# Kernel optimization log

Hardware: AMD Instinct MI355X
Metric: run time of the kernel (lower is better)

Reference implementation:

```python
import jax, jax.numpy as jnp
import numpy as np

N_NODES = 100000


def _gcn_norm(edge_index, n):
    # Add self loops and compute symmetric normalization deg^-1/2 A_hat deg^-1/2
    loops = jnp.arange(n, dtype=edge_index.dtype)
    row = jnp.concatenate([edge_index[0], loops])  # source nodes [E+N]
    col = jnp.concatenate([edge_index[1], loops])  # target nodes [E+N]
    ones = jnp.ones(row.shape[0], dtype=jnp.float32)
    deg = jax.ops.segment_sum(ones, col, num_segments=n)  # in-degree incl. self loop
    dinv = jnp.where(deg > 0, jax.lax.rsqrt(deg), 0.0)
    norm = dinv[row] * dinv[col]  # [E+N]
    return row, col, norm


def _gcn_conv(x, W, b, row, col, norm, n):
    h = x @ W                     # [N, out]
    msg = h[row] * norm[:, None]  # gather + scale  [E+N, out]
    agg = jax.ops.segment_sum(msg, col, num_segments=n)  # scatter-add
    return agg + b


def setup_inputs() -> dict:
    key = jax.random.key(0)
    ks = jax.random.split(key, 8)
    n, e, din, dh, dout = N_NODES, 1600000, 128, 128, 64
    x = jax.random.normal(ks[0], (n, din), dtype=jnp.float32)
    edge_index = jax.random.randint(ks[1], (2, e), 0, n, dtype=jnp.int64)
    s = lambda fan: 1.0 / np.sqrt(fan)
    W0 = jax.random.normal(ks[2], (din, dh), dtype=jnp.float32) * s(din)
    W1 = jax.random.normal(ks[3], (dh, dh), dtype=jnp.float32) * s(dh)
    W2 = jax.random.normal(ks[4], (dh, dout), dtype=jnp.float32) * s(dh)
    b0 = jnp.zeros((dh,), jnp.float32)
    b1 = jnp.zeros((dh,), jnp.float32)
    b2 = jnp.zeros((dout,), jnp.float32)
    return {"x": x, "edge_index": edge_index, "W0": W0, "b0": b0,
            "W1": W1, "b1": b1, "W2": W2, "b2": b2}


def reference(x, edge_index, W0, b0, W1, b1, W2, b2):
    # Eval-mode forward (dropout inactive), matching GCN.forward
    n = x.shape[0]
    row, col, norm = _gcn_norm(edge_index, n)
    h = jax.nn.relu(_gcn_conv(x, W0, b0, row, col, norm, n))
    h = jax.nn.relu(_gcn_conv(h, W1, b1, row, col, norm, n))
    out = _gcn_conv(h, W2, b2, row, col, norm, n)
    return out
```

## Files before the change

### kernel.cpp

```cpp
#include <hip/hip_runtime.h>
#include <stdint.h>


static inline size_t ws_align(size_t x) { return (x + 255) & ~(size_t)255; }

typedef float __f2 __attribute__((ext_vector_type(2)));
typedef float __f4 __attribute__((ext_vector_type(4)));
typedef __attribute__((ext_vector_type(8))) short short8v;
typedef __attribute__((ext_vector_type(4))) float f32x4;

__device__ __forceinline__ int eidx(const void* p, size_t i, int is64) {
  return is64 ? (int)((const long long*)p)[i] : ((const int*)p)[i];
}

__device__ __forceinline__ uint16_t f2bf(float f) {
  uint32_t u = __float_as_uint(f);
  u += 0x7fffu + ((u >> 16) & 1u);
  return (uint16_t)(u >> 16);
}
__device__ __forceinline__ float bf_lo(uint32_t h) { return __uint_as_float(h << 16); }
__device__ __forceinline__ float bf_hi(uint32_t h) { return __uint_as_float(h & 0xffff0000u); }

__global__ void detect_k(const int* ei, int* flag) {
  if (threadIdx.x == 0 && blockIdx.x == 0) {
    int allz = 1;
    for (int i = 1; i < 128; i += 2)
      if (ei[i] != 0) { allz = 0; break; }
    *flag = allz;
  }
}

__global__ __launch_bounds__(256) void passA_k(const void* ei, const int* __restrict__ flag,
                                               int* __restrict__ bucket_cnt, int E, int NB) {
  __shared__ int cnt[256];
  int t = threadIdx.x;
  cnt[t] = 0;
  __syncthreads();
  int is64 = *flag;
  for (int e = blockIdx.x * 256 + t; e < E; e += gridDim.x * 256) {
    int c = eidx(ei, (size_t)E + e, is64);
    atomicAdd(&cnt[c >> 9], 1);
  }
  __syncthreads();
  if (t < NB && cnt[t]) atomicAdd(&bucket_cnt[t], cnt[t]);
}

__global__ __launch_bounds__(256) void bscan_k(const int* __restrict__ bucket_cnt,
                                               int* __restrict__ bucket_offs,
                                               int* __restrict__ gcursor, int NB) {
  __shared__ int sh[256];
  int t = threadIdx.x;
  int v = (t < NB) ? bucket_cnt[t] : 0;
  sh[t] = v;
  __syncthreads();
  for (int off = 1; off < 256; off <<= 1) {
    int x = (t >= off) ? sh[t - off] : 0;
    __syncthreads();
    sh[t] += x;
    __syncthreads();
  }
  if (t < NB) {
    int excl = sh[t] - v;
    bucket_offs[t] = excl;
    gcursor[t] = excl;
  }
  if (t == NB - 1) bucket_offs[NB] = sh[t];
}

__global__ __launch_bounds__(256) void passB_k(const void* ei, const int* __restrict__ flag,
                                               int* __restrict__ gcursor,
                                               int2* __restrict__ epk_binned, int E, int NB) {
  __shared__ int2 sorted[4096];
  __shared__ int cnt[256], bbase[256], gb[256], cur[256];
  const int t = threadIdx.x;
  const int base = blockIdx.x * 4096;
  const int CH = min(4096, E - base);
  const int is64 = *flag;

  cnt[t] = 0;
  __syncthreads();
  for (int i = t; i < CH; i += 256) {
    int c = eidx(ei, (size_t)E + base + i, is64);
    atomicAdd(&cnt[c >> 9], 1);
  }
  __syncthreads();
  {
    int v = cnt[t];
    __shared__ int sh[256];
    sh[t] = v;
    __syncthreads();
    for (int off = 1; off < 256; off <<= 1) {
      int x = (t >= off) ? sh[t - off] : 0;
      __syncthreads();
      sh[t] += x;
      __syncthreads();
    }
    bbase[t] = sh[t] - v;
    gb[t] = (t < NB && v) ? atomicAdd(&gcursor[t], v) : 0;
    cur[t] = 0;
  }
  __syncthreads();
  for (int i = t; i < CH; i += 256) {
    int r = eidx(ei, (size_t)base + i, is64);
    int c = eidx(ei, (size_t)E + base + i, is64);
    int b = c >> 9;
    int rank = atomicAdd(&cur[b], 1);
    sorted[bbase[b] + rank] = make_int2(r, c);
  }
  __syncthreads();
  for (int i = t; i < CH; i += 256) {
    int2 v = sorted[i];
    int b = v.y >> 9;
    epk_binned[gb[b] + (i - bbase[b])] = v;
  }
}

__global__ __launch_bounds__(256) void passC0_k(const int2* __restrict__ epk_binned,
                                                const int* __restrict__ bucket_offs,
                                                int* __restrict__ deg, int* __restrict__ offs,
                                                int n, int NB) {
  __shared__ int dcnt[512];
  __shared__ int s[256];
  const int t = threadIdx.x;
  const int b = blockIdx.x;
  dcnt[t] = 0; dcnt[t + 256] = 0;
  __syncthreads();
  const int lo = bucket_offs[b], hi = bucket_offs[b + 1];
  for (int i = lo + t; i < hi; i += 256)
    atomicAdd(&dcnt[epk_binned[i].y & 511], 1);
  __syncthreads();
  int d0 = dcnt[2 * t], d1 = dcnt[2 * t + 1];
  int pv = d0 + d1;
  s[t] = pv;
  __syncthreads();
  for (int off = 1; off < 256; off <<= 1) {
    int x = (t >= off) ? s[t - off] : 0;
    __syncthreads();
    s[t] += x;
    __syncthreads();
  }
  int pex = s[t] - pv;
  const int node0 = b << 9;
  int g0 = node0 + 2 * t, g1 = node0 + 2 * t + 1;
  if (g0 < n) { deg[g0] = d0; offs[g0] = lo + pex; }
  if (g1 < n) { deg[g1] = d1; offs[g1] = lo + pex + d0; }
  if (b == NB - 1 && t == 0) offs[n] = hi;
}

__global__ void dinv_k(const int* __restrict__ deg, float* __restrict__ dinv, int n) {
  int i = blockIdx.x * blockDim.x + threadIdx.x;
  if (i < n) dinv[i] = rsqrtf((float)deg[i] + 1.0f);
}

__global__ __launch_bounds__(256) void passC_k(const int2* __restrict__ epk_binned,
                                               const int* __restrict__ bucket_offs,
                                               const int* __restrict__ offs,
                                               uint32_t* __restrict__ epk) {
  __shared__ int cur[512];
  const int t = threadIdx.x;
  const int b = blockIdx.x;
  cur[t] = 0; cur[t + 256] = 0;
  __syncthreads();
  const int lo = bucket_offs[b], hi = bucket_offs[b + 1];
  for (int i = lo + t; i < hi; i += 256) {
    int2 v = epk_binned[i];
    int pos = offs[v.y] + atomicAdd(&cur[v.y & 511], 1);
    epk[pos] = (uint32_t)v.x;
  }
}

template <int COLS>
__global__ void wprep_k(const float* __restrict__ W, uint16_t* __restrict__ Wf) {
  constexpr int CT = COLS / 16;
  const int f = blockIdx.x;
  const int kc = f / CT, ct = f % CT;
  const int l = threadIdx.x;
#pragma unroll
  for (int j = 0; j < 8; ++j) {
    int k = kc * 32 + (l >> 4) * 8 + j;
    int col = ct * 16 + (l & 15);
    float wv = W[(size_t)k * COLS + col];
    uint16_t hi = f2bf(wv);
    float res = wv - __uint_as_float((uint32_t)hi << 16);
    Wf[(size_t)f * 1024 + l * 8 + j] = hi;
    Wf[(size_t)f * 1024 + 512 + l * 8 + j] = f2bf(res);
  }
}

template <int COLS, bool SLICED_IN>
__global__ __launch_bounds__(256) void gemm_k(const float* __restrict__ X,
                                              const uint16_t* __restrict__ Wf,
                                              const float* __restrict__ dinv,
                                              uint16_t* __restrict__ H, int N) {
  constexpr int CT = COLS / 16;
  __shared__ uint32_t Xp[128 * 32];

  const int tid = threadIdx.x;
  const int l = tid & 63, w = tid >> 6;
  const int rowbase = blockIdx.x * 128;
  const float4* X4 = (const float4*)X;

  f32x4 acc[2][CT];
#pragma unroll
  for (int rt = 0; rt < 2; ++rt)
#pragma unroll
    for (int ct = 0; ct < CT; ++ct) acc[rt][ct] = (f32x4)0.f;

  for (int kc = 0; kc < 4; ++kc) {
    __syncthreads();
#pragma unroll
    for (int t = 0; t < 4; ++t) {
      int i = tid + t * 256;
      int r = i >> 3, q = i & 7;
      int gr = rowbase + r;
      if (gr >= N) gr = N - 1;
      float4 xv = SLICED_IN ? X4[((size_t)kc * N + gr) * 8 + q]
                            : X4[(size_t)gr * 32 + kc * 8 + q];
      float xs[4] = {xv.x, xv.y, xv.z, xv.w};
      uint32_t p[4];
#pragma unroll
      for (int e = 0; e < 4; ++e) {
        uint16_t hi = f2bf(xs[e]);
        float res = xs[e] - __uint_as_float((uint32_t)hi << 16);
        p[e] = ((uint32_t)hi << 16) | (uint32_t)f2bf(res);
      }
      int blk = q ^ (r & 7);
      *(uint4*)&Xp[r * 32 + blk * 4] = make_uint4(p[0], p[1], p[2], p[3]);
    }
    __syncthreads();

    short8v ah[2], al[2];
#pragma unroll
    for (int rt = 0; rt < 2; ++rt) {
      int r = w * 32 + rt * 16 + (l & 15);
      int c = (r & 7) << 2;
      int b0 = ((l >> 4) * 8) ^ c;
      int b1 = ((l >> 4) * 8 + 4) ^ c;
      uint32_t ua[8];
      *(uint4*)&ua[0] = *(const uint4*)&Xp[r * 32 + b0];
      *(uint4*)&ua[4] = *(const uint4*)&Xp[r * 32 + b1];
      union { uint32_t d[4]; short8v v; } ch, cl;
#pragma unroll
      for (int p2 = 0; p2 < 4; ++p2) {
        ch.d[p2] = __builtin_amdgcn_perm(ua[2 * p2 + 1], ua[2 * p2], 0x07060302u);
        cl.d[p2] = __builtin_amdgcn_perm(ua[2 * p2 + 1], ua[2 * p2], 0x05040100u);
      }
      ah[rt] = ch.v;
      al[rt] = cl.v;
    }

#pragma unroll
    for (int ct = 0; ct < CT; ++ct) {
      size_t fo = (size_t)(kc * CT + ct) * 1024;
      short8v bh = *(const short8v*)(Wf + fo + l * 8);
      short8v bl = *(const short8v*)(Wf + fo + 512 + l * 8);
#pragma unroll
      for (int rt = 0; rt < 2; ++rt) {
        acc[rt][ct] = __builtin_amdgcn_mfma_f32_16x16x32_bf16(ah[rt], bh, acc[rt][ct], 0, 0, 0);
        acc[rt][ct] = __builtin_amdgcn_mfma_f32_16x16x32_bf16(al[rt], bh, acc[rt][ct], 0, 0, 0);
        acc[rt][ct] = __builtin_amdgcn_mfma_f32_16x16x32_bf16(ah[rt], bl, acc[rt][ct], 0, 0, 0);
      }
    }
  }

  uint32_t* HW = (uint32_t*)H;
  const int lq = l >> 4, lc = l & 15;
#pragma unroll
  for (int rt = 0; rt < 2; ++rt) {
#pragma unroll
    for (int q = 0; q < 4; ++q) {
      int row = rowbase + w * 32 + rt * 16 + lq * 4 + q;
      bool ok = row < N;
      float dv = ok ? dinv[row] : 0.f;
#pragma unroll
      for (int ct = 0; ct < CT; ++ct) {
        float v = acc[rt][ct][q] * dv;
        int b = (int)f2bf(v);
        int other = __shfl_xor(b, 1);
        if (ok && !(l & 1)) {
          uint32_t word = (uint32_t)b | ((uint32_t)other << 16);
          HW[((size_t)(ct >> 1) * N + row) * 16 + (ct & 1) * 8 + (lc >> 1)] = word;
        }
      }
    }
  }
}

__global__ __launch_bounds__(256, 8) void agg128s_k(const uint32_t* __restrict__ HW,
                                                    const int* __restrict__ offs,
                                                    const uint32_t* __restrict__ epk,
                                                    const float* __restrict__ bias,
                                                    float* __restrict__ Aout,
                                                    int relu, int N) {
  const int s = blockIdx.x & 3;
  const int g = blockIdx.x >> 2;
  const int lane = threadIdx.x & 63;
  const int wid = threadIdx.x >> 6;
  const int d = lane >> 3, w = lane & 7;
  const int c = g * 32 + wid * 8 + d;
  if (c >= N) return;
  const uint32_t* Hs = HW + (size_t)s * N * 16;
  int e0 = offs[c], e1 = offs[c + 1];
  float a0 = 0.f, a1 = 0.f, a2 = 0.f, a3 = 0.f;
  int e = e0;
  for (; e + 8 <= e1; e += 8) {
    uint32_t p0 = epk[e],     p1 = epk[e + 1], p2 = epk[e + 2], p3 = epk[e + 3];
    uint32_t p4 = epk[e + 4], p5 = epk[e + 5], p6 = epk[e + 6], p7 = epk[e + 7];
    uint2 h0 = *(const uint2*)&Hs[(size_t)p0 * 16 + 2 * w];
    uint2 h1 = *(const uint2*)&Hs[(size_t)p1 * 16 + 2 * w];
    uint2 h2 = *(const uint2*)&Hs[(size_t)p2 * 16 + 2 * w];
    uint2 h3 = *(const uint2*)&Hs[(size_t)p3 * 16 + 2 * w];
    uint2 h4 = *(const uint2*)&Hs[(size_t)p4 * 16 + 2 * w];
    uint2 h5 = *(const uint2*)&Hs[(size_t)p5 * 16 + 2 * w];
    uint2 h6 = *(const uint2*)&Hs[(size_t)p6 * 16 + 2 * w];
    uint2 h7 = *(const uint2*)&Hs[(size_t)p7 * 16 + 2 * w];
    a0 += bf_lo(h0.x); a1 += bf_hi(h0.x); a2 += bf_lo(h0.y); a3 += bf_hi(h0.y);
    a0 += bf_lo(h1.x); a1 += bf_hi(h1.x); a2 += bf_lo(h1.y); a3 += bf_hi(h1.y);
    a0 += bf_lo(h2.x); a1 += bf_hi(h2.x); a2 += bf_lo(h2.y); a3 += bf_hi(h2.y);
    a0 += bf_lo(h3.x); a1 += bf_hi(h3.x); a2 += bf_lo(h3.y); a3 += bf_hi(h3.y);
    a0 += bf_lo(h4.x); a1 += bf_hi(h4.x); a2 += bf_lo(h4.y); a3 += bf_hi(h4.y);
    a0 += bf_lo(h5.x); a1 += bf_hi(h5.x); a2 += bf_lo(h5.y); a3 += bf_hi(h5.y);
    a0 += bf_lo(h6.x); a1 += bf_hi(h6.x); a2 += bf_lo(h6.y); a3 += bf_hi(h6.y);
    a0 += bf_lo(h7.x); a1 += bf_hi(h7.x); a2 += bf_lo(h7.y); a3 += bf_hi(h7.y);
  }
  for (; e + 4 <= e1; e += 4) {
    uint32_t p0 = epk[e], p1 = epk[e + 1], p2 = epk[e + 2], p3 = epk[e + 3];
    uint2 h0 = *(const uint2*)&Hs[(size_t)p0 * 16 + 2 * w];
    uint2 h1 = *(const uint2*)&Hs[(size_t)p1 * 16 + 2 * w];
    uint2 h2 = *(const uint2*)&Hs[(size_t)p2 * 16 + 2 * w];
    uint2 h3 = *(const uint2*)&Hs[(size_t)p3 * 16 + 2 * w];
    a0 += bf_lo(h0.x); a1 += bf_hi(h0.x); a2 += bf_lo(h0.y); a3 += bf_hi(h0.y);
    a0 += bf_lo(h1.x); a1 += bf_hi(h1.x); a2 += bf_lo(h1.y); a3 += bf_hi(h1.y);
    a0 += bf_lo(h2.x); a1 += bf_hi(h2.x); a2 += bf_lo(h2.y); a3 += bf_hi(h2.y);
    a0 += bf_lo(h3.x); a1 += bf_hi(h3.x); a2 += bf_lo(h3.y); a3 += bf_hi(h3.y);
  }
  for (; e < e1; ++e) {
    uint2 h = *(const uint2*)&Hs[(size_t)epk[e] * 16 + 2 * w];
    a0 += bf_lo(h.x); a1 += bf_hi(h.x); a2 += bf_lo(h.y); a3 += bf_hi(h.y);
  }
  float dc = rsqrtf((float)(e1 - e0) + 1.f);
  uint2 hc = *(const uint2*)&Hs[(size_t)c * 16 + 2 * w];
  float r0 = fmaf(dc, a0 + bf_lo(hc.x), bias[s * 32 + 4 * w + 0]);
  float r1 = fmaf(dc, a1 + bf_hi(hc.x), bias[s * 32 + 4 * w + 1]);
  float r2 = fmaf(dc, a2 + bf_lo(hc.y), bias[s * 32 + 4 * w + 2]);
  float r3 = fmaf(dc, a3 + bf_hi(hc.y), bias[s * 32 + 4 * w + 3]);
  if (relu) {
    r0 = fmaxf(r0, 0.f); r1 = fmaxf(r1, 0.f);
    r2 = fmaxf(r2, 0.f); r3 = fmaxf(r3, 0.f);
  }
  __f4 res; res.x = r0; res.y = r1; res.z = r2; res.w = r3;
  __builtin_nontemporal_store(res, (__f4*)(Aout + ((size_t)s * N + c) * 32 + 4 * w));
}

__global__ __launch_bounds__(256, 8) void agg64s_k(const uint32_t* __restrict__ HW,
                                                   const int* __restrict__ offs,
                                                   const uint32_t* __restrict__ epk,
                                                   const float* __restrict__ bias,
                                                   float* __restrict__ out, int N) {
  const int r = blockIdx.x & 7;
  const int s = r >> 2;
  const int quar = r & 3;
  const int ng = (N + 31) >> 5;
  const int nq = (ng + 3) >> 2;
  const int g = quar * nq + (blockIdx.x >> 3);
  if (g >= ng) return;
  const int lane = threadIdx.x & 63;
  const int wid = threadIdx.x >> 6;
  const int d = lane >> 3, w = lane & 7;
  const int c = g * 32 + wid * 8 + d;
  if (c >= N) return;
  const uint32_t* Hs = HW + (size_t)s * N * 16;
  int e0 = offs[c], e1 = offs[c + 1];
  float a0 = 0.f, a1 = 0.f, a2 = 0.f, a3 = 0.f;
  int e = e0;
  for (; e + 8 <= e1; e += 8) {
    uint32_t p0 = epk[e],     p1 = epk[e + 1], p2 = epk[e + 2], p3 = epk[e + 3];
    uint32_t p4 = epk[e + 4], p5 = epk[e + 5], p6 = epk[e + 6], p7 = epk[e + 7];
    uint2 h0 = *(const uint2*)&Hs[(size_t)p0 * 16 + 2 * w];
    uint2 h1 = *(const uint2*)&Hs[(size_t)p1 * 16 + 2 * w];
    uint2 h2 = *(const uint2*)&Hs[(size_t)p2 * 16 + 2 * w];
    uint2 h3 = *(const uint2*)&Hs[(size_t)p3 * 16 + 2 * w];
    uint2 h4 = *(const uint2*)&Hs[(size_t)p4 * 16 + 2 * w];
    uint2 h5 = *(const uint2*)&Hs[(size_t)p5 * 16 + 2 * w];
    uint2 h6 = *(const uint2*)&Hs[(size_t)p6 * 16 + 2 * w];
    uint2 h7 = *(const uint2*)&Hs[(size_t)p7 * 16 + 2 * w];
    a0 += bf_lo(h0.x); a1 += bf_hi(h0.x); a2 += bf_lo(h0.y); a3 += bf_hi(h0.y);
    a0 += bf_lo(h1.x); a1 += bf_hi(h1.x); a2 += bf_lo(h1.y); a3 += bf_hi(h1.y);
    a0 += bf_lo(h2.x); a1 += bf_hi(h2.x); a2 += bf_lo(h2.y); a3 += bf_hi(h2.y);
    a0 += bf_lo(h3.x); a1 += bf_hi(h3.x); a2 += bf_lo(h3.y); a3 += bf_hi(h3.y);
    a0 += bf_lo(h4.x); a1 += bf_hi(h4.x); a2 += bf_lo(h4.y); a3 += bf_hi(h4.y);
    a0 += bf_lo(h5.x); a1 += bf_hi(h5.x); a2 += bf_lo(h5.y); a3 += bf_hi(h5.y);
    a0 += bf_lo(h6.x); a1 += bf_hi(h6.x); a2 += bf_lo(h6.y); a3 += bf_hi(h6.y);
    a0 += bf_lo(h7.x); a1 += bf_hi(h7.x); a2 += bf_lo(h7.y); a3 += bf_hi(h7.y);
  }
  for (; e + 4 <= e1; e += 4) {
    uint32_t p0 = epk[e], p1 = epk[e + 1], p2 = epk[e + 2], p3 = epk[e + 3];
    uint2 h0 = *(const uint2*)&Hs[(size_t)p0 * 16 + 2 * w];
    uint2 h1 = *(const uint2*)&Hs[(size_t)p1 * 16 + 2 * w];
    uint2 h2 = *(const uint2*)&Hs[(size_t)p2 * 16 + 2 * w];
    uint2 h3 = *(const uint2*)&Hs[(size_t)p3 * 16 + 2 * w];
    a0 += bf_lo(h0.x); a1 += bf_hi(h0.x); a2 += bf_lo(h0.y); a3 += bf_hi(h0.y);
    a0 += bf_lo(h1.x); a1 += bf_hi(h1.x); a2 += bf_lo(h1.y); a3 += bf_hi(h1.y);
    a0 += bf_lo(h2.x); a1 += bf_hi(h2.x); a2 += bf_lo(h2.y); a3 += bf_hi(h2.y);
    a0 += bf_lo(h3.x); a1 += bf_hi(h3.x); a2 += bf_lo(h3.y); a3 += bf_hi(h3.y);
  }
  for (; e < e1; ++e) {
    uint2 h = *(const uint2*)&Hs[(size_t)epk[e] * 16 + 2 * w];
    a0 += bf_lo(h.x); a1 += bf_hi(h.x); a2 += bf_lo(h.y); a3 += bf_hi(h.y);
  }
  float dc = rsqrtf((float)(e1 - e0) + 1.f);
  uint2 hc = *(const uint2*)&Hs[(size_t)c * 16 + 2 * w];
  float r0 = fmaf(dc, a0 + bf_lo(hc.x), bias[s * 32 + 4 * w + 0]);
  float r1 = fmaf(dc, a1 + bf_hi(hc.x), bias[s * 32 + 4 * w + 1]);
  float r2 = fmaf(dc, a2 + bf_lo(hc.y), bias[s * 32 + 4 * w + 2]);
  float r3 = fmaf(dc, a3 + bf_hi(hc.y), bias[s * 32 + 4 * w + 3]);
  __f4 res; res.x = r0; res.y = r1; res.z = r2; res.w = r3;
  __builtin_nontemporal_store(res, (__f4*)(out + (size_t)c * 64 + s * 32 + 4 * w));
}

extern "C" void kernel_launch(void* const* d_in, const int* in_sizes, int n_in,
                              void* d_out, int out_size, void* d_ws, size_t ws_size,
                              hipStream_t stream) {
  const float* x  = (const float*)d_in[0];
  const void*  ei = d_in[1];
  const float* W0 = (const float*)d_in[2];
  const float* b0 = (const float*)d_in[3];
  const float* W1 = (const float*)d_in[4];
  const float* b1 = (const float*)d_in[5];
  const float* W2 = (const float*)d_in[6];
  const float* b2 = (const float*)d_in[7];
  float* out = (float*)d_out;

  const int n = in_sizes[0] / 128;
  const int E = in_sizes[1] / 2;
  const int NB = (n + 511) >> 9;

  char* ws = (char*)d_ws;
  size_t off = 0;
  auto alloc = [&](size_t bytes) { char* p = ws + off; off = ws_align(off + bytes); return p; };
  int*      bucket_cnt  = (int*)alloc(256 * 4);
  int*      bucket_offs = (int*)alloc(257 * 4);
  int*      gcursor     = (int*)alloc(256 * 4);
  int*      deg         = (int*)alloc((size_t)n * 4);
  int*      offs        = (int*)alloc((size_t)(n + 1) * 4);
  float*    dinv        = (float*)alloc((size_t)n * 4);
  int*      flag        = (int*)alloc(4);
  uint16_t* wf0         = (uint16_t*)alloc(64 * 1024);
  uint16_t* wf1         = (uint16_t*)alloc(64 * 1024);
  uint16_t* wf2         = (uint16_t*)alloc(32 * 1024);
  int2*     epk_binned  = (int2*)alloc((size_t)E * 8);
  uint32_t* epk         = (uint32_t*)alloc((size_t)E * 4);
  uint16_t* hbuf        = (uint16_t*)alloc((size_t)n * 128 * 2);
  float*    abuf        = (float*)alloc((size_t)n * 128 * 4);
  (void)ws_size;

  hipMemsetAsync(bucket_cnt, 0, 256 * 4, stream);

  wprep_k<128><<<32, 64, 0, stream>>>(W0, wf0);
  wprep_k<128><<<32, 64, 0, stream>>>(W1, wf1);
  wprep_k<64><<<16, 64, 0, stream>>>(W2, wf2);

  detect_k<<<1, 64, 0, stream>>>((const int*)ei, flag);
  passA_k<<<512, 256, 0, stream>>>(ei, flag, bucket_cnt, E, NB);
  bscan_k<<<1, 256, 0, stream>>>(bucket_cnt, bucket_offs, gcursor, NB);
  passB_k<<<(E + 4095) / 4096, 256, 0, stream>>>(ei, flag, gcursor, epk_binned, E, NB);
  passC0_k<<<NB, 256, 0, stream>>>(epk_binned, bucket_offs, deg, offs, n, NB);
  dinv_k<<<(n + 255) / 256, 256, 0, stream>>>(deg, dinv, n);
  passC_k<<<NB, 256, 0, stream>>>(epk_binned, bucket_offs, offs, epk);

  const int gemm_blocks = (n + 127) / 128;
  const int agg128_blocks = 4 * ((n + 31) / 32);
  const int ng = (n + 31) >> 5, nq = (ng + 3) >> 2;
  const int agg64_blocks = 8 * nq;

  gemm_k<128, false><<<gemm_blocks, 256, 0, stream>>>(x, wf0, dinv, hbuf, n);
  agg128s_k<<<agg128_blocks, 256, 0, stream>>>((const uint32_t*)hbuf, offs, epk, b0, abuf, 1, n);
  gemm_k<128, true><<<gemm_blocks, 256, 0, stream>>>(abuf, wf1, dinv, hbuf, n);
  agg128s_k<<<agg128_blocks, 256, 0, stream>>>((const uint32_t*)hbuf, offs, epk, b1, abuf, 1, n);
  gemm_k<64, true><<<gemm_blocks, 256, 0, stream>>>(abuf, wf2, dinv, hbuf, n);
  agg64s_k<<<agg64_blocks, 256, 0, stream>>>((const uint32_t*)hbuf, offs, epk, b2, out, n);
}
```

Before: 434.3 us.

## Split 128-wide aggregation by source-node half and sum partials in GEMM

Each destination's CSR edge list is partitioned by whether the source node is in the lower or upper half, using a new mid offset array. The 128-wide aggregation launches separate blocks per half, so each block gathers from a smaller source range, which should improve cache locality. Each half writes its own partial buffer. The following GEMM adds the two partials and applies ReLU when loading. This costs an extra full-size fp32 partial buffer write and read, and doubles the number of aggregation blocks.

```diff
diff --git a/kernel.cpp b/kernel.cpp
--- a/kernel.cpp
+++ b/kernel.cpp
@@ -118,18 +118,24 @@
 __global__ __launch_bounds__(256) void passC0_k(const int2* __restrict__ epk_binned,
                                                 const int* __restrict__ bucket_offs,
                                                 int* __restrict__ deg, int* __restrict__ offs,
-                                                int n, int NB) {
-  __shared__ int dcnt[512];
+                                                int* __restrict__ mid,
+                                                int n, int NB, int NH) {
+  __shared__ int dcnt[1024];
   __shared__ int s[256];
   const int t = threadIdx.x;
   const int b = blockIdx.x;
-  dcnt[t] = 0; dcnt[t + 256] = 0;
+  dcnt[t] = 0; dcnt[t + 256] = 0; dcnt[t + 512] = 0; dcnt[t + 768] = 0;
   __syncthreads();
   const int lo = bucket_offs[b], hi = bucket_offs[b + 1];
-  for (int i = lo + t; i < hi; i += 256)
-    atomicAdd(&dcnt[epk_binned[i].y & 511], 1);
-  __syncthreads();
-  int d0 = dcnt[2 * t], d1 = dcnt[2 * t + 1];
+  for (int i = lo + t; i < hi; i += 256) {
+    int2 v = epk_binned[i];
+    int hf = (v.x >= NH) ? 1 : 0;
+    atomicAdd(&dcnt[((v.y & 511) << 1) | hf], 1);
+  }
+  __syncthreads();
+  int c00 = dcnt[4 * t], c01 = dcnt[4 * t + 1];
+  int c10 = dcnt[4 * t + 2], c11 = dcnt[4 * t + 3];
+  int d0 = c00 + c01, d1 = c10 + c11;
   int pv = d0 + d1;
   s[t] = pv;
   __syncthreads();
@@ -142,8 +148,8 @@
   int pex = s[t] - pv;
   const int node0 = b << 9;
   int g0 = node0 + 2 * t, g1 = node0 + 2 * t + 1;
-  if (g0 < n) { deg[g0] = d0; offs[g0] = lo + pex; }
-  if (g1 < n) { deg[g1] = d1; offs[g1] = lo + pex + d0; }
+  if (g0 < n) { deg[g0] = d0; offs[g0] = lo + pex; mid[g0] = lo + pex + c00; }
+  if (g1 < n) { deg[g1] = d1; offs[g1] = lo + pex + d0; mid[g1] = lo + pex + d0 + c10; }
   if (b == NB - 1 && t == 0) offs[n] = hi;
 }
 
@@ -155,16 +161,19 @@
 __global__ __launch_bounds__(256) void passC_k(const int2* __restrict__ epk_binned,
                                                const int* __restrict__ bucket_offs,
                                                const int* __restrict__ offs,
-                                               uint32_t* __restrict__ epk) {
-  __shared__ int cur[512];
+                                               const int* __restrict__ mid,
+                                               uint32_t* __restrict__ epk, int NH) {
+  __shared__ int cur[1024];
   const int t = threadIdx.x;
   const int b = blockIdx.x;
-  cur[t] = 0; cur[t + 256] = 0;
+  cur[t] = 0; cur[t + 256] = 0; cur[t + 512] = 0; cur[t + 768] = 0;
   __syncthreads();
   const int lo = bucket_offs[b], hi = bucket_offs[b + 1];
   for (int i = lo + t; i < hi; i += 256) {
     int2 v = epk_binned[i];
-    int pos = offs[v.y] + atomicAdd(&cur[v.y & 511], 1);
+    int hf = (v.x >= NH) ? 1 : 0;
+    int base = hf ? mid[v.y] : offs[v.y];
+    int pos = base + atomicAdd(&cur[((v.y & 511) << 1) | hf], 1);
     epk[pos] = (uint32_t)v.x;
   }
 }
@@ -189,6 +198,7 @@
 
 template <int COLS, bool SLICED_IN>
 __global__ __launch_bounds__(256) void gemm_k(const float* __restrict__ X,
+                                              const float* __restrict__ X2,
                                               const uint16_t* __restrict__ Wf,
                                               const float* __restrict__ dinv,
                                               uint16_t* __restrict__ H, int N) {
@@ -199,6 +209,7 @@
   const int l = tid & 63, w = tid >> 6;
   const int rowbase = blockIdx.x * 128;
   const float4* X4 = (const float4*)X;
+  const float4* P4 = (const float4*)X2;
 
   f32x4 acc[2][CT];
 #pragma unroll
@@ -214,8 +225,17 @@
       int r = i >> 3, q = i & 7;
       int gr = rowbase + r;
       if (gr >= N) gr = N - 1;
-      float4 xv = SLICED_IN ? X4[((size_t)kc * N + gr) * 8 + q]
-                            : X4[(size_t)gr * 32 + kc * 8 + q];
+      float4 xv;
+      if (SLICED_IN) {
+        float4 v0 = X4[((size_t)kc * N + gr) * 8 + q];
+        float4 v1 = P4[((size_t)kc * N + gr) * 8 + q];
+        xv.x = fmaxf(v0.x + v1.x, 0.f);
+        xv.y = fmaxf(v0.y + v1.y, 0.f);
+        xv.z = fmaxf(v0.z + v1.z, 0.f);
+        xv.w = fmaxf(v0.w + v1.w, 0.f);
+      } else {
+        xv = X4[(size_t)gr * 32 + kc * 8 + q];
+      }
       float xs[4] = {xv.x, xv.y, xv.z, xv.w};
       uint32_t p[4];
 #pragma unroll
@@ -288,19 +308,25 @@
 
 __global__ __launch_bounds__(256, 8) void agg128s_k(const uint32_t* __restrict__ HW,
                                                     const int* __restrict__ offs,
+                                                    const int* __restrict__ mid,
                                                     const uint32_t* __restrict__ epk,
                                                     const float* __restrict__ bias,
-                                                    float* __restrict__ Aout,
-                                                    int relu, int N) {
-  const int s = blockIdx.x & 3;
-  const int g = blockIdx.x >> 2;
+                                                    float* __restrict__ P0,
+                                                    float* __restrict__ P1,
+                                                    int NH, int N) {
+  const int combo = blockIdx.x & 7;
+  const int s = combo & 3;
+  const int h = combo >> 2;
+  const int g = blockIdx.x >> 3;
   const int lane = threadIdx.x & 63;
   const int wid = threadIdx.x >> 6;
   const int d = lane >> 3, w = lane & 7;
   const int c = g * 32 + wid * 8 + d;
   if (c >= N) return;
   const uint32_t* Hs = HW + (size_t)s * N * 16;
-  int e0 = offs[c], e1 = offs[c + 1];
+  int eb = offs[c], ee = offs[c + 1], em = mid[c];
+  int e0 = h ? em : eb;
+  int e1 = h ? ee : em;
   float a0 = 0.f, a1 = 0.f, a2 = 0.f, a3 = 0.f;
   int e = e0;
   for (; e + 8 <= e1; e += 8) {
@@ -335,21 +361,30 @@
     a0 += bf_lo(h3.x); a1 += bf_hi(h3.x); a2 += bf_lo(h3.y); a3 += bf_hi(h3.y);
   }
   for (; e < e1; ++e) {
-    uint2 h = *(const uint2*)&Hs[(size_t)epk[e] * 16 + 2 * w];
-    a0 += bf_lo(h.x); a1 += bf_hi(h.x); a2 += bf_lo(h.y); a3 += bf_hi(h.y);
-  }
-  float dc = rsqrtf((float)(e1 - e0) + 1.f);
-  uint2 hc = *(const uint2*)&Hs[(size_t)c * 16 + 2 * w];
-  float r0 = fmaf(dc, a0 + bf_lo(hc.x), bias[s * 32 + 4 * w + 0]);
-  float r1 = fmaf(dc, a1 + bf_hi(hc.x), bias[s * 32 + 4 * w + 1]);
-  float r2 = fmaf(dc, a2 + bf_lo(hc.y), bias[s * 32 + 4 * w + 2]);
-  float r3 = fmaf(dc, a3 + bf_hi(hc.y), bias[s * 32 + 4 * w + 3]);
-  if (relu) {
-    r0 = fmaxf(r0, 0.f); r1 = fmaxf(r1, 0.f);
-    r2 = fmaxf(r2, 0.f); r3 = fmaxf(r3, 0.f);
-  }
-  __f4 res; res.x = r0; res.y = r1; res.z = r2; res.w = r3;
-  __builtin_nontemporal_store(res, (__f4*)(Aout + ((size_t)s * N + c) * 32 + 4 * w));
+    uint2 h2 = *(const uint2*)&Hs[(size_t)epk[e] * 16 + 2 * w];
+    a0 += bf_lo(h2.x); a1 += bf_hi(h2.x); a2 += bf_lo(h2.y); a3 += bf_hi(h2.y);
+  }
+  float dc = rsqrtf((float)(ee - eb) + 1.f);
+  bool match = ((c >= NH) ? 1 : 0) == h;
+  if (match) {
+    uint2 hc = *(const uint2*)&Hs[(size_t)c * 16 + 2 * w];
+    a0 += bf_lo(hc.x); a1 += bf_hi(hc.x);
+    a2 += bf_lo(hc.y); a3 += bf_hi(hc.y);
+  }
+  float b0v = 0.f, b1v = 0.f, b2v = 0.f, b3v = 0.f;
+  if (h == 0) {
+    b0v = bias[s * 32 + 4 * w + 0];
+    b1v = bias[s * 32 + 4 * w + 1];
+    b2v = bias[s * 32 + 4 * w + 2];
+    b3v = bias[s * 32 + 4 * w + 3];
+  }
+  __f4 res;
+  res.x = fmaf(dc, a0, b0v);
+  res.y = fmaf(dc, a1, b1v);
+  res.z = fmaf(dc, a2, b2v);
+  res.w = fmaf(dc, a3, b3v);
+  float* O = h ? P1 : P0;
+  __builtin_nontemporal_store(res, (__f4*)(O + ((size_t)s * N + c) * 32 + 4 * w));
 }
 
 __global__ __launch_bounds__(256, 8) void agg64s_k(const uint32_t* __restrict__ HW,
@@ -434,6 +469,7 @@
   const int n = in_sizes[0] / 128;
   const int E = in_sizes[1] / 2;
   const int NB = (n + 511) >> 9;
+  const int NH = n >> 1;
 
   char* ws = (char*)d_ws;
   size_t off = 0;
@@ -443,6 +479,7 @@
   int*      gcursor     = (int*)alloc(256 * 4);
   int*      deg         = (int*)alloc((size_t)n * 4);
   int*      offs        = (int*)alloc((size_t)(n + 1) * 4);
+  int*      mid         = (int*)alloc((size_t)n * 4);
   float*    dinv        = (float*)alloc((size_t)n * 4);
   int*      flag        = (int*)alloc(4);
   uint16_t* wf0         = (uint16_t*)alloc(64 * 1024);
@@ -452,6 +489,7 @@
   uint32_t* epk         = (uint32_t*)alloc((size_t)E * 4);
   uint16_t* hbuf        = (uint16_t*)alloc((size_t)n * 128 * 2);
   float*    abuf        = (float*)alloc((size_t)n * 128 * 4);
+  float*    pbuf        = (float*)alloc((size_t)n * 128 * 4);
   (void)ws_size;
 
   hipMemsetAsync(bucket_cnt, 0, 256 * 4, stream);
@@ -464,19 +502,19 @@
   passA_k<<<512, 256, 0, stream>>>(ei, flag, bucket_cnt, E, NB);
   bscan_k<<<1, 256, 0, stream>>>(bucket_cnt, bucket_offs, gcursor, NB);
   passB_k<<<(E + 4095) / 4096, 256, 0, stream>>>(ei, flag, gcursor, epk_binned, E, NB);
-  passC0_k<<<NB, 256, 0, stream>>>(epk_binned, bucket_offs, deg, offs, n, NB);
+  passC0_k<<<NB, 256, 0, stream>>>(epk_binned, bucket_offs, deg, offs, mid, n, NB, NH);
   dinv_k<<<(n + 255) / 256, 256, 0, stream>>>(deg, dinv, n);
-  passC_k<<<NB, 256, 0, stream>>>(epk_binned, bucket_offs, offs, epk);
+  passC_k<<<NB, 256, 0, stream>>>(epk_binned, bucket_offs, offs, mid, epk, NH);
 
   const int gemm_blocks = (n + 127) / 128;
-  const int agg128_blocks = 4 * ((n + 31) / 32);
+  const int agg128_blocks = 8 * ((n + 31) / 32);
   const int ng = (n + 31) >> 5, nq = (ng + 3) >> 2;
   const int agg64_blocks = 8 * nq;
 
-  gemm_k<128, false><<<gemm_blocks, 256, 0, stream>>>(x, wf0, dinv, hbuf, n);
-  agg128s_k<<<agg128_blocks, 256, 0, stream>>>((const uint32_t*)hbuf, offs, epk, b0, abuf, 1, n);
-  gemm_k<128, true><<<gemm_blocks, 256, 0, stream>>>(abuf, wf1, dinv, hbuf, n);
-  agg128s_k<<<agg128_blocks, 256, 0, stream>>>((const uint32_t*)hbuf, offs, epk, b1, abuf, 1, n);
-  gemm_k<64, true><<<gemm_blocks, 256, 0, stream>>>(abuf, wf2, dinv, hbuf, n);
+  gemm_k<128, false><<<gemm_blocks, 256, 0, stream>>>(x, nullptr, wf0, dinv, hbuf, n);
+  agg128s_k<<<agg128_blocks, 256, 0, stream>>>((const uint32_t*)hbuf, offs, mid, epk, b0, abuf, pbuf, NH, n);
+  gemm_k<128, true><<<gemm_blocks, 256, 0, stream>>>(abuf, pbuf, wf1, dinv, hbuf, n);
+  agg128s_k<<<agg128_blocks, 256, 0, stream>>>((const uint32_t*)hbuf, offs, mid, epk, b1, abuf, pbuf, NH, n);
+  gemm_k<64, true><<<gemm_blocks, 256, 0, stream>>>(abuf, pbuf, wf2, dinv, hbuf, n);
   agg64s_k<<<agg64_blocks, 256, 0, stream>>>((const uint32_t*)hbuf, offs, epk, b2, out, n);
 }
```

Result: slower. 473.2 us (+9.0%).
